# Performance work log

Measured on AMD Instinct MI355X. Metric: run time of the kernel, lower is better.

The kernel has to match this reference:

```python
import jax, jax.numpy as jnp
import numpy as np

E = 40000   # num_entities
R = 474     # num_relations
D = 200     # Config.embedding_dim
L = 100     # n_num_lit
B = 32      # batch

def setup_inputs() -> dict:
    key = jax.random.key(0)
    ks = jax.random.split(key, 11)
    return {
        "e1": jax.random.randint(ks[0], (B, 1), 0, E),
        "rel": jax.random.randint(ks[1], (B, 1), 0, R),
        "emb_e": jax.random.normal(ks[2], (E, D), jnp.float32) * 0.1,           # emb_e.weight
        "emb_rel": jax.random.normal(ks[3], (R, D), jnp.float32) * 0.1,         # emb_rel.weight
        "num_lit": jax.random.normal(ks[4], (E, L), jnp.float32),               # numerical_literals (raw)
        "num_lit_norm": jax.random.uniform(ks[5], (E, L), jnp.float32),         # numerical_literals_normalized
        "W_lit": jax.random.normal(ks[6], (D, D + L), jnp.float32) / np.float32(np.sqrt(D + L)),  # emb_num_lit.weight
        "b_lit": jnp.zeros((D,), jnp.float32),                                  # emb_num_lit.bias
        "c": jax.random.normal(ks[7], (L,), jnp.float32),                       # RBF centers (fixed)
        "var": jax.random.uniform(ks[8], (L,), jnp.float32, minval=0.5, maxval=2.0),  # RBF variances (fixed)
        "nf_w": jax.random.normal(ks[9], (R, L), jnp.float32) * 0.1,            # nf_weights.weight
    }

def reference(e1, rel, emb_e, emb_rel, num_lit, num_lit_norm, W_lit, b_lit, c, var, nf_w):
    e1f = e1.reshape(-1)    # (B,)
    relf = rel.reshape(-1)  # (B,)
    # LiteralE gating via linear layer: emb_num_lit(cat([emb, lit]))
    e1_emb = jnp.concatenate([emb_e[e1f], num_lit_norm[e1f]], axis=1) @ W_lit.T + b_lit  # (B, D)
    e2_multi_emb = jnp.concatenate([emb_e, num_lit_norm], axis=1) @ W_lit.T + b_lit      # (E, D)
    rel_emb = emb_rel[relf]                                                              # (B, D)
    # dropout is identity at inference
    score_l = (e1_emb * rel_emb) @ e2_multi_emb.T  # (B, E)
    # KBLN numerical-literal score: broadcast diff + RBF + weighted reduction over literals
    n = num_lit[e1f][:, None, :] - num_lit[None, :, :]   # (B, E, L) -- large intermediate
    phi = jnp.exp(-jnp.square(n - c) / var)              # RBF, pointwise
    score_n = jnp.einsum('bel,bl->be', phi, nf_w[relf])  # bmm(phi, w_nf^T).squeeze()
    return jax.nn.sigmoid(score_l + score_n)             # (B, E)
```

## Files before the change

kernel.cpp:

```cpp
#include <hip/hip_runtime.h>
#include <math.h>

#define E_N 40000
#define D_N 200
#define L_N 100
#define K_N 300
#define B_N 32

typedef float  f32x4 __attribute__((ext_vector_type(4)));
typedef short  s16x8 __attribute__((ext_vector_type(8)));

#define WS_SH 0
#define WS_W  3200
#define WS_NR 6400
#define WS_S0 6500
#define WS_PA 6532

#define SM_W    1600
#define SM_NR   3200
#define SM_CB   3316
#define SM_TOT  3828

__device__ inline float fast_exp2(float x) {
#if __has_builtin(__builtin_amdgcn_exp2f)
    return __builtin_amdgcn_exp2f(x);
#else
    return exp2f(x);
#endif
}
__device__ inline float fast_rcp(float x) {
#if __has_builtin(__builtin_amdgcn_rcpf)
    return __builtin_amdgcn_rcpf(x);
#else
    return 1.0f / x;
#endif
}
__device__ inline ushort f2bf(float f) {
    uint u = __builtin_bit_cast(uint, f);
    u += 0x7fffu + ((u >> 16) & 1u);
    return (ushort)(u >> 16);
}
__device__ inline s16x8 pack_bf8(f32x4 lo, f32x4 hi) {
    s16x8 bb;
    bb[0] = (short)f2bf(lo[0]); bb[1] = (short)f2bf(lo[1]);
    bb[2] = (short)f2bf(lo[2]); bb[3] = (short)f2bf(lo[3]);
    bb[4] = (short)f2bf(hi[0]); bb[5] = (short)f2bf(hi[1]);
    bb[6] = (short)f2bf(hi[2]); bb[7] = (short)f2bf(hi[3]);
    return bb;
}

__global__ __launch_bounds__(320) void prep_kernel(
    const int* __restrict__ e1, const int* __restrict__ rel,
    const float* __restrict__ emb_e, const float* __restrict__ emb_rel,
    const float* __restrict__ num_lit, const float* __restrict__ num_lit_norm,
    const float* __restrict__ W, const float* __restrict__ b_lit,
    const float* __restrict__ c, const float* __restrict__ var,
    const float* __restrict__ nf_w, float* __restrict__ ws)
{
    const int b = blockIdx.x;
    const int t = threadIdx.x;
    __shared__ float q[D_N];
    const int e1b = e1[b];
    const int rb  = rel[b];

    if (t < D_N) {
        const float* wr = W + t * K_N;
        const float* er = emb_e + (long)e1b * D_N;
        const float* nl = num_lit_norm + (long)e1b * L_N;
        float s0_ = b_lit[t], s1_ = 0.f, s2_ = 0.f, s3_ = 0.f;
        for (int k = 0; k < D_N; k += 4) {
            s0_ += er[k+0] * wr[k+0]; s1_ += er[k+1] * wr[k+1];
            s2_ += er[k+2] * wr[k+2]; s3_ += er[k+3] * wr[k+3];
        }
        for (int k = 0; k < L_N; k += 4) {
            s0_ += nl[k+0] * wr[D_N+k+0]; s1_ += nl[k+1] * wr[D_N+k+1];
            s2_ += nl[k+2] * wr[D_N+k+2]; s3_ += nl[k+3] * wr[D_N+k+3];
        }
        q[t] = ((s0_ + s1_) + (s2_ + s3_)) * emb_rel[rb * D_N + t];
    }
    __syncthreads();

    {
        float pk = 0.f;
        if (t < K_N) {
            float a0 = 0.f, a1 = 0.f, a2 = 0.f, a3 = 0.f;
            for (int d = 0; d < D_N; d += 4) {
                a0 += q[d+0] * W[(d+0) * K_N + t];
                a1 += q[d+1] * W[(d+1) * K_N + t];
                a2 += q[d+2] * W[(d+2) * K_N + t];
                a3 += q[d+3] * W[(d+3) * K_N + t];
            }
            pk = (a0 + a1) + (a2 + a3);
        }
        const int s  = t >> 5;
        const int g  = (t >> 3) & 3;
        const int j  = t & 7;
        const int mt = b >> 4;
        const int ln = (g << 4) | (b & 15);
        ushort* pa = (ushort*)(ws + WS_PA);
        pa[((mt * 10 + s) * 64 + ln) * 8 + j] = f2bf(pk);
    }

    if (t < L_N) {
        const float r = sqrtf(1.4426950408889634f / var[t]);
        ws[WS_SH + t * 32 + b] = r * (num_lit[(long)e1b * L_N + t] - c[t]);
        ws[WS_W  + t * 32 + b] = nf_w[rb * L_N + t];
        if (b == 0) ws[WS_NR + t] = -r;
    }
    if (t == 300) {
        float s = 0.f;
        for (int d = 0; d < D_N; ++d) s += q[d] * b_lit[d];
        ws[WS_S0 + b] = s;
    }
}

__global__ __launch_bounds__(256, 4) void score_kernel(
    const float* __restrict__ emb_e, const float* __restrict__ num_lit,
    const float* __restrict__ num_lit_norm, const float* __restrict__ ws,
    float* __restrict__ out)
{
    __shared__ float smem[SM_TOT];

    const int lane = threadIdx.x & 63;
    const int wv   = threadIdx.x >> 6;
    const int wti  = wv & 1;
    const int h    = wv >> 1;
    const int mt   = blockIdx.x & 1;
    const int egp  = blockIdx.x >> 1;
    const int eg   = egp * 2 + wti;
    const int er   = lane & 15;
    const int g    = lane >> 4;
    const int e    = eg * 16 + er;
    const int mt4  = mt * 4;

    {
        const f32x4* s4 = (const f32x4*)ws;
        f32x4* d4 = (f32x4*)smem;
        for (int i = threadIdx.x; i < 829; i += 256) {
            int src;
            if (i < 400) {
                src = (i >> 2) * 8 + mt4 + (i & 3);
            } else if (i < 800) {
                const int ii = i - 400;
                src = 800 + (ii >> 2) * 8 + mt4 + (ii & 3);
            } else if (i < 825) {
                src = 1600 + (i - 800);
            } else {
                src = 1625 + mt4 + (i - 825);
            }
            d4[i] = s4[src];
        }
    }

    f32x4 acc = {0.f, 0.f, 0.f, 0.f};
    if (h == 0) acc = *(const f32x4*)(ws + WS_S0 + mt * 16 + 4 * g);

    s16x8 afr[5];
    {
        const s16x8* pAg = (const s16x8*)(ws + WS_PA);
#pragma unroll
        for (int i = 0; i < 5; ++i) afr[i] = pAg[(mt * 10 + h * 5 + i) * 64 + lane];
    }

    const float* embr = emb_e        + (long)e * D_N;
    const float* litn = num_lit_norm + (long)e * L_N;

#pragma unroll
    for (int i = 0; i < 4; ++i) {
        const int k0 = 32 * (h * 5 + i) + 8 * g;
        const float* bp = (k0 < 200) ? (embr + k0) : (litn + (k0 - 200));
        f32x4 lo = *(const f32x4*)bp;
        f32x4 hi = *(const f32x4*)(bp + 4);
        acc = __builtin_amdgcn_mfma_f32_16x16x32_bf16(afr[i], pack_bf8(lo, hi), acc, 0, 0, 0);
    }
    if (h == 0) {
        const int k0 = 128 + 8 * g;
        f32x4 lo = *(const f32x4*)(embr + k0);
        f32x4 hi = *(const f32x4*)(embr + k0 + 4);
        acc = __builtin_amdgcn_mfma_f32_16x16x32_bf16(afr[4], pack_bf8(lo, hi), acc, 0, 0, 0);
    } else {
        f32x4 z = {0.f, 0.f, 0.f, 0.f};
        f32x4 lo = z, hi = z;
        if (g == 0)      { lo = *(const f32x4*)(litn + 88); hi = *(const f32x4*)(litn + 92); }
        else if (g == 1) { lo = *(const f32x4*)(litn + 96); }
        acc = __builtin_amdgcn_mfma_f32_16x16x32_bf16(afr[4], pack_bf8(lo, hi), acc, 0, 0, 0);
    }

    __syncthreads();

    const float* shT = smem;
    const float* wT  = smem + SM_W;
    const f32x4* n4  = (const f32x4*)(smem + SM_NR);

    const int lc0 = h ? 13 : 0;
    const int lcE = h ? 25 : 13;
    const f32x4* m4 = (const f32x4*)(num_lit + (long)e * L_N);
    f32x4 mv_a = m4[lc0];
    f32x4 mv_b = m4[lc0 + 1];
    for (int lc = lc0; lc < lcE; ++lc) {
        const f32x4 mv = mv_a;
        mv_a = mv_b;
        if (lc + 2 < lcE) mv_b = m4[lc + 2];
        f32x4 nv = n4[lc];
#pragma unroll
        for (int ll = 0; ll < 4; ++ll) {
            const int l = lc * 4 + ll;
            const float rm = nv[ll] * mv[ll];
            f32x4 s4v = *(const f32x4*)(shT + l * 16 + 4 * g);
            f32x4 w4v = *(const f32x4*)(wT  + l * 16 + 4 * g);
#pragma unroll
            for (int j = 0; j < 4; ++j) {
                const float u = rm + s4v[j];
                acc[j] = fmaf(fast_exp2(-(u * u)), w4v[j], acc[j]);
            }
        }
    }

    float* cbuf = smem + SM_CB;
    if (h) {
        *(f32x4*)(cbuf + (wti * 64 + lane) * 4) = acc;
    }
    __syncthreads();
    if (!h) {
        const f32x4 o = *(const f32x4*)(cbuf + (wti * 64 + lane) * 4);
#pragma unroll
        for (int j = 0; j < 4; ++j) {
            const float v = acc[j] + o[j];
            const float z = fast_exp2(v * -1.4426950408889634f);
            out[(long)(mt * 16 + 4 * g + j) * E_N + e] = fast_rcp(1.0f + z);
        }
    }
}

extern "C" void kernel_launch(void* const* d_in, const int* in_sizes, int n_in,
                              void* d_out, int out_size, void* d_ws, size_t ws_size,
                              hipStream_t stream) {
    const int*   e1       = (const int*)d_in[0];
    const int*   rel      = (const int*)d_in[1];
    const float* emb_e    = (const float*)d_in[2];
    const float* emb_rel  = (const float*)d_in[3];
    const float* num_lit  = (const float*)d_in[4];
    const float* num_lit_norm = (const float*)d_in[5];
    const float* W_lit    = (const float*)d_in[6];
    const float* b_lit    = (const float*)d_in[7];
    const float* c        = (const float*)d_in[8];
    const float* var      = (const float*)d_in[9];
    const float* nf_w     = (const float*)d_in[10];
    float* out = (float*)d_out;
    float* ws  = (float*)d_ws;

    hipLaunchKernelGGL(prep_kernel, dim3(B_N), dim3(320), 0, stream,
                       e1, rel, emb_e, emb_rel, num_lit, num_lit_norm,
                       W_lit, b_lit, c, var, nf_w, ws);
    hipLaunchKernelGGL(score_kernel, dim3(2500), dim3(256), 0, stream,
                       emb_e, num_lit, num_lit_norm, ws, out);
}
```

Before: 48.82 us.

## Remap score blocks so one block covers all 32 batch rows for 16 entities

Each block previously handled two entity groups for one half of the batch. It now handles one entity group for both batch halves, with the two waves per half split by mt instead of by entity group. Shared memory stages the full workspace (all 32 batch columns) in one straight copy, replacing the indexed gather, and the barrier moves before the MFMA stage. The same entity rows of emb_e and num_lit are now loaded by both mt waves within one block, which may improve cache reuse. In exchange LDS use roughly doubles, which can lower occupancy, and the early barrier removes the overlap between the staging copy and the MFMA loads.

```diff
diff --git a/kernel.cpp b/kernel.cpp
--- a/kernel.cpp
+++ b/kernel.cpp
@@ -16,10 +16,8 @@
 #define WS_S0 6500
 #define WS_PA 6532
 
-#define SM_W    1600
-#define SM_NR   3200
-#define SM_CB   3316
-#define SM_TOT  3828
+#define SM_CB  6532
+#define SM_TOT 7044
 
 __device__ inline float fast_exp2(float x) {
 #if __has_builtin(__builtin_amdgcn_exp2f)
@@ -123,37 +121,23 @@
 
     const int lane = threadIdx.x & 63;
     const int wv   = threadIdx.x >> 6;
-    const int wti  = wv & 1;
+    const int mt   = wv & 1;
     const int h    = wv >> 1;
-    const int mt   = blockIdx.x & 1;
-    const int egp  = blockIdx.x >> 1;
-    const int eg   = egp * 2 + wti;
+    const int eg   = blockIdx.x;
     const int er   = lane & 15;
     const int g    = lane >> 4;
     const int e    = eg * 16 + er;
-    const int mt4  = mt * 4;
+    const int b0   = mt * 16 + 4 * g;
 
     {
         const f32x4* s4 = (const f32x4*)ws;
         f32x4* d4 = (f32x4*)smem;
-        for (int i = threadIdx.x; i < 829; i += 256) {
-            int src;
-            if (i < 400) {
-                src = (i >> 2) * 8 + mt4 + (i & 3);
-            } else if (i < 800) {
-                const int ii = i - 400;
-                src = 800 + (ii >> 2) * 8 + mt4 + (ii & 3);
-            } else if (i < 825) {
-                src = 1600 + (i - 800);
-            } else {
-                src = 1625 + mt4 + (i - 825);
-            }
-            d4[i] = s4[src];
-        }
-    }
+        for (int i = threadIdx.x; i < 1633; i += 256) d4[i] = s4[i];
+    }
+    __syncthreads();
 
     f32x4 acc = {0.f, 0.f, 0.f, 0.f};
-    if (h == 0) acc = *(const f32x4*)(ws + WS_S0 + mt * 16 + 4 * g);
+    if (h == 0) acc = *(const f32x4*)(ws + WS_S0 + b0);
 
     s16x8 afr[5];
     {
@@ -186,12 +170,6 @@
         acc = __builtin_amdgcn_mfma_f32_16x16x32_bf16(afr[4], pack_bf8(lo, hi), acc, 0, 0, 0);
     }
 
-    __syncthreads();
-
-    const float* shT = smem;
-    const float* wT  = smem + SM_W;
-    const f32x4* n4  = (const f32x4*)(smem + SM_NR);
-
     const int lc0 = h ? 13 : 0;
     const int lcE = h ? 25 : 13;
     const f32x4* m4 = (const f32x4*)(num_lit + (long)e * L_N);
@@ -201,13 +179,13 @@
         const f32x4 mv = mv_a;
         mv_a = mv_b;
         if (lc + 2 < lcE) mv_b = m4[lc + 2];
-        f32x4 nv = n4[lc];
+        const f32x4 nv = *(const f32x4*)(smem + WS_NR + lc * 4);
 #pragma unroll
         for (int ll = 0; ll < 4; ++ll) {
             const int l = lc * 4 + ll;
             const float rm = nv[ll] * mv[ll];
-            f32x4 s4v = *(const f32x4*)(shT + l * 16 + 4 * g);
-            f32x4 w4v = *(const f32x4*)(wT  + l * 16 + 4 * g);
+            f32x4 s4v = *(const f32x4*)(smem + WS_SH + l * 32 + b0);
+            f32x4 w4v = *(const f32x4*)(smem + WS_W  + l * 32 + b0);
 #pragma unroll
             for (int j = 0; j < 4; ++j) {
                 const float u = rm + s4v[j];
@@ -218,16 +196,16 @@
 
     float* cbuf = smem + SM_CB;
     if (h) {
-        *(f32x4*)(cbuf + (wti * 64 + lane) * 4) = acc;
+        *(f32x4*)(cbuf + (mt * 64 + lane) * 4) = acc;
     }
     __syncthreads();
     if (!h) {
-        const f32x4 o = *(const f32x4*)(cbuf + (wti * 64 + lane) * 4);
+        const f32x4 o = *(const f32x4*)(cbuf + (mt * 64 + lane) * 4);
 #pragma unroll
         for (int j = 0; j < 4; ++j) {
             const float v = acc[j] + o[j];
             const float z = fast_exp2(v * -1.4426950408889634f);
-            out[(long)(mt * 16 + 4 * g + j) * E_N + e] = fast_rcp(1.0f + z);
+            out[(long)(b0 + j) * E_N + e] = fast_rcp(1.0f + z);
         }
     }
 }
```

Result: faster. 46.58 us (-4.6%).
